# Performance work log

Measured on AMD Instinct MI355X. Metric: run time of the kernel, lower is better.

## Reference

```python
import jax, jax.numpy as jnp
import numpy as np

NW, L, D, H = 4096, 64, 128, 8
HD = D // H  # 16
NEG = -1e9


def setup_inputs() -> dict:
    key = jax.random.key(0)
    k1, k2, k3, k4, k5, k6, k7 = jax.random.split(key, 7)
    feat = jax.random.normal(k1, (NW, L, D), dtype=jnp.float32)
    pos = jax.random.normal(k2, (NW, L, D), dtype=jnp.float32) * 0.1
    # ragged window occupancy: lengths in [1, L]; mask True = padded key
    lengths = jax.random.randint(k3, (NW,), 1, L + 1)
    mask = jnp.arange(L)[None, :] >= lengths[:, None]  # [NW, L] bool
    in_proj_w = jax.random.normal(k4, (3 * D, D), dtype=jnp.float32) * 0.05
    in_proj_b = jax.random.normal(k5, (3 * D,), dtype=jnp.float32) * 0.02
    out_w = jax.random.normal(k6, (D, D), dtype=jnp.float32) * 0.05
    out_b = jax.random.normal(k7, (D,), dtype=jnp.float32) * 0.02
    return {"feat": feat, "pos": pos, "mask": mask, "in_proj_w": in_proj_w,
            "in_proj_b": in_proj_b, "out_w": out_w, "out_b": out_b}


def reference(feat, pos, mask, in_proj_w, in_proj_b, out_w, out_b):
    # q = k = feat + pos, v = feat (positional bias only on q/k, as in source)
    qk_in = feat + pos  # [NW, L, D]
    Wq, Wk, Wv = in_proj_w[:D], in_proj_w[D:2 * D], in_proj_w[2 * D:]
    bq, bk, bv = in_proj_b[:D], in_proj_b[D:2 * D], in_proj_b[2 * D:]
    q = (qk_in @ Wq.T + bq).reshape(NW, L, H, HD)
    k = (qk_in @ Wk.T + bk).reshape(NW, L, H, HD)
    v = (feat @ Wv.T + bv).reshape(NW, L, H, HD)
    scale = 1.0 / np.sqrt(HD)
    scores = jnp.einsum('nqhd,nkhd->nhqk', q, k) * scale  # [NW, H, L, L]
    scores = jnp.where(mask[:, None, None, :], NEG, scores)
    attn = jax.nn.softmax(scores, axis=-1)
    ctx = jnp.einsum('nhqk,nkhd->nqhd', attn, v).reshape(NW, L, D)
    return ctx @ out_w.T + out_b  # [NW, L, D]
```

## Files before the change

kernel.cpp:

```cpp
#include <hip/hip_runtime.h>
#include <hip/hip_bf16.h>

#define NWIN 4096
#define LW   64
#define DIM  128

typedef __attribute__((ext_vector_type(8))) short bf8;
typedef __attribute__((ext_vector_type(4))) float f4;

#define MFMA(a,b,c) __builtin_amdgcn_mfma_f32_16x16x32_bf16((a),(b),(c),0,0,0)

__device__ __forceinline__ unsigned short bfr(float f){
  __hip_bfloat16 h = __float2bfloat16(f);
  union { __hip_bfloat16 h; unsigned short u; } x; x.h = h; return x.u;
}
__device__ __forceinline__ unsigned long long pack4f(float a,float b,float c,float d){
  float2 lo2; lo2.x = a; lo2.y = b;
  float2 hi2; hi2.x = c; hi2.y = d;
  union { __hip_bfloat162 h[2]; unsigned long long u; } x;
  x.h[0] = __float22bfloat162_rn(lo2);
  x.h[1] = __float22bfloat162_rn(hi2);
  return x.u;
}
__device__ __forceinline__ bf8 mk_bf8(unsigned long long lo, unsigned long long hi){
  union { unsigned long long q[2]; bf8 v; } u; u.q[0]=lo; u.q[1]=hi; return u.v;
}

__device__ __forceinline__ bf8 frag_lds(const char* sm, int off, int rs,
                                        int rowBase, int kb, int l15, int lq){
  int row = rowBase + l15;
  int sw = (row & 7) << 4;
  unsigned long long lo = *(const unsigned long long*)(sm + off + row*rs + ((kb + 8*lq) ^ sw));
  unsigned long long hi = *(const unsigned long long*)(sm + off + row*rs + ((kb + 8*lq + 32) ^ sw));
  union { unsigned long long q[2]; bf8 v; } u; u.q[0]=lo; u.q[1]=hi; return u.v;
}

__global__ void detect_mask_kernel(const unsigned char* __restrict__ mask,
                                   int* __restrict__ ws){
  int t = blockIdx.x * blockDim.x + threadIdx.x;
  int local = 0;
  for (int i = t; i < NWIN * LW; i += gridDim.x * blockDim.x)
    if ((i & 3) && mask[i]) local = 1;
  if (local) atomicOr(ws, 1);
}

__global__ void wfrag_kernel(const float* __restrict__ in_w,
                             const float* __restrict__ ow,
                             unsigned short* __restrict__ dst){
  int t = blockIdx.x * blockDim.x + threadIdx.x;
  if (t >= 4*4*8*64*8) return;
  int e  = t & 7;
  int l  = (t >> 3) & 63;
  int nt = (t >> 9) & 7;
  int kt = (t >> 12) & 3;
  int p  = t >> 14;
  int k = kt*32 + 4*(l >> 4) + (e & 3) + 16*(e >> 2);
  int n = nt*16 + (l & 15);
  float v = (p < 3) ? in_w[(p*128 + n)*128 + k] : ow[n*128 + k];
  dst[t] = bfr(v);
}

__launch_bounds__(256, 4)
__global__ void win_attn_mfma(const float* __restrict__ feat,
                              const float* __restrict__ pos,
                              const float* __restrict__ in_b,
                              const float* __restrict__ ob,
                              const unsigned char* __restrict__ maskb,
                              const int* __restrict__ wsflag,
                              const unsigned short* __restrict__ wf,
                              float* __restrict__ out){
  extern __shared__ char sm[];
  const int n    = blockIdx.x;
  const int tid  = threadIdx.x;
  const int wave = tid >> 6, lane = tid & 63, l15 = lane & 15, lq = lane >> 4;

  const int B0 = 0, B1 = 16384;
  const f4 fzero = {0.f, 0.f, 0.f, 0.f};

  const float* fb = feat + (size_t)n * (LW*DIM);
  const float* pb = pos  + (size_t)n * (LW*DIM);
  #pragma unroll
  for (int it = 0; it < 8; ++it){
    int j = tid + it*256; int r = j >> 5, q = j & 31;
    float4 f = *(const float4*)(fb + r*DIM + q*4);
    float4 p = *(const float4*)(pb + r*DIM + q*4);
    int sw = (r & 7) << 4;
    *(unsigned long long*)(sm + B1 + r*256 + ((q*8) ^ sw)) = pack4f(f.x, f.y, f.z, f.w);
    *(unsigned long long*)(sm + B0 + r*256 + ((q*8) ^ sw)) =
        pack4f(f.x + p.x, f.y + p.y, f.z + p.z, f.w + p.w);
  }
  int mv = wsflag[0] ? (int)maskb[(size_t)n*LW + lane]
                     : ((const int*)maskb)[(size_t)n*LW + lane];
  unsigned long long bal = __ballot(mv != 0);
  const int len = bal ? (int)__builtin_ctzll(bal) : LW;
  float4 bq4[2], bk4[2];
  #pragma unroll
  for (int hh = 0; hh < 2; ++hh){
    int h = wave + 4*hh;
    bq4[hh] = *(const float4*)(in_b + h*16 + 4*lq);
    bk4[hh] = *(const float4*)(in_b + 128 + h*16 + 4*lq);
  }
  __syncthreads();

  unsigned long long q8lo[2][4], k8lo[2][4];
  {
    f4 qT[2][4], kT[2][4];
    #pragma unroll
    for (int hh = 0; hh < 2; ++hh)
      #pragma unroll
      for (int nt = 0; nt < 4; ++nt){ qT[hh][nt] = fzero; kT[hh][nt] = fzero; }
    #pragma unroll
    for (int kt = 0; kt < 4; ++kt){
      bf8 wq[2], wk[2];
      #pragma unroll
      for (int hh = 0; hh < 2; ++hh){
        int h = wave + 4*hh;
        wq[hh] = *(const bf8*)(wf + (size_t)(((0*4 + kt)*8 + h)*64 + lane)*8);
        wk[hh] = *(const bf8*)(wf + (size_t)(((1*4 + kt)*8 + h)*64 + lane)*8);
      }
      bf8 x[4];
      #pragma unroll
      for (int nt = 0; nt < 4; ++nt)
        x[nt] = frag_lds(sm, B0, 256, nt*16, kt*64, l15, lq);
      #pragma unroll
      for (int hh = 0; hh < 2; ++hh)
        #pragma unroll
        for (int nt = 0; nt < 4; ++nt){
          qT[hh][nt] = MFMA(wq[hh], x[nt], qT[hh][nt]);
          kT[hh][nt] = MFMA(wk[hh], x[nt], kT[hh][nt]);
        }
    }
    #pragma unroll
    for (int hh = 0; hh < 2; ++hh)
      #pragma unroll
      for (int nt = 0; nt < 4; ++nt){
        q8lo[hh][nt] = pack4f((qT[hh][nt][0] + bq4[hh].x) * 0.25f,
                              (qT[hh][nt][1] + bq4[hh].y) * 0.25f,
                              (qT[hh][nt][2] + bq4[hh].z) * 0.25f,
                              (qT[hh][nt][3] + bq4[hh].w) * 0.25f);
        k8lo[hh][nt] = pack4f(kT[hh][nt][0] + bk4[hh].x,
                              kT[hh][nt][1] + bk4[hh].y,
                              kT[hh][nt][2] + bk4[hh].z,
                              kT[hh][nt][3] + bk4[hh].w);
      }
  }

  f4 aV[2][4];
  #pragma unroll
  for (int g = 0; g < 2; ++g)
    #pragma unroll
    for (int nt = 0; nt < 4; ++nt) aV[g][nt] = fzero;
  #pragma unroll
  for (int kt = 0; kt < 4; ++kt){
    bf8 wv[2];
    #pragma unroll
    for (int g = 0; g < 2; ++g){
      int mt = wave + 4*g;
      wv[g] = *(const bf8*)(wf + (size_t)(((2*4 + kt)*8 + mt)*64 + lane)*8);
    }
    bf8 xf[4];
    #pragma unroll
    for (int nt = 0; nt < 4; ++nt)
      xf[nt] = frag_lds(sm, B1, 256, nt*16, kt*64, l15, lq);
    #pragma unroll
    for (int g = 0; g < 2; ++g)
      #pragma unroll
      for (int nt = 0; nt < 4; ++nt)
        aV[g][nt] = MFMA(wv[g], xf[nt], aV[g][nt]);
  }
  __syncthreads();

  #pragma unroll
  for (int g = 0; g < 2; ++g){
    int mt = wave + 4*g;
    #pragma unroll
    for (int r = 0; r < 4; ++r){
      int dim = mt*16 + 4*lq + r;
      float bv_ = in_b[256 + dim];
      #pragma unroll
      for (int nt = 0; nt < 4; ++nt){
        int col = nt*16 + l15;
        *(unsigned short*)(sm + B0 + dim*128 + ((col*2) ^ ((dim&7)<<4))) =
            bfr(aV[g][nt][r] + bv_);
      }
    }
  }

  const unsigned long long qhi = (lq == 0) ? 0x3f80ull : 0ull;
  unsigned long long khi[4];
  #pragma unroll
  for (int mt = 0; mt < 4; ++mt){
    float mval = (mt*16 + l15 < len) ? 0.f : -1e9f;
    khi[mt] = (lq == 0) ? (unsigned long long)bfr(mval) : 0ull;
  }

  #pragma unroll
  for (int hh = 0; hh < 2; ++hh){
    int h = wave + 4*hh;
    bf8 av0 = frag_lds(sm, B0, 128, h*16, 0,  l15, lq);
    bf8 av1 = frag_lds(sm, B0, 128, h*16, 64, l15, lq);
    #pragma unroll
    for (int nh = 0; nh < 2; ++nh){
      f4 s[4][2];
      __builtin_amdgcn_s_setprio(1);
      #pragma unroll
      for (int mt = 0; mt < 4; ++mt)
        #pragma unroll
        for (int j = 0; j < 2; ++j)
          s[mt][j] = MFMA(mk_bf8(k8lo[hh][mt], khi[mt]),
                          mk_bf8(q8lo[hh][2*nh + j], qhi), fzero);
      __builtin_amdgcn_s_setprio(0);
      float inv[2];
      #pragma unroll
      for (int j = 0; j < 2; ++j){
        float ss = 0.f;
        #pragma unroll
        for (int mt = 0; mt < 4; ++mt)
          #pragma unroll
          for (int r = 0; r < 4; ++r){
            float p = __expf(s[mt][j][r]);
            s[mt][j][r] = p;
            ss += p;
          }
        ss += __shfl_xor(ss, 16);
        ss += __shfl_xor(ss, 32);
        inv[j] = __builtin_amdgcn_rcpf(ss);
      }
      bf8 pb_[2][2];
      #pragma unroll
      for (int kt = 0; kt < 2; ++kt)
        #pragma unroll
        for (int j = 0; j < 2; ++j){
          unsigned long long lo = pack4f(s[2*kt  ][j][0], s[2*kt  ][j][1],
                                         s[2*kt  ][j][2], s[2*kt  ][j][3]);
          unsigned long long hi = pack4f(s[2*kt+1][j][0], s[2*kt+1][j][1],
                                         s[2*kt+1][j][2], s[2*kt+1][j][3]);
          union { unsigned long long q[2]; bf8 v; } u; u.q[0]=lo; u.q[1]=hi;
          pb_[kt][j] = u.v;
        }
      __builtin_amdgcn_s_setprio(1);
      #pragma unroll
      for (int j = 0; j < 2; ++j){
        f4 c = fzero;
        c = MFMA(av0, pb_[0][j], c);
        c = MFMA(av1, pb_[1][j], c);
        int row = (2*nh + j)*16 + l15;
        unsigned long long w = pack4f(c[0]*inv[j], c[1]*inv[j],
                                      c[2]*inv[j], c[3]*inv[j]);
        *(unsigned long long*)(sm + B1 + row*256 +
            ((32*h + 8*lq) ^ ((row&7)<<4))) = w;
      }
      __builtin_amdgcn_s_setprio(0);
    }
  }
  __syncthreads();

  {
    f4 acc[4][2];
    #pragma unroll
    for (int mt = 0; mt < 4; ++mt)
      #pragma unroll
      for (int g = 0; g < 2; ++g) acc[mt][g] = fzero;
    #pragma unroll
    for (int kt = 0; kt < 4; ++kt){
      bf8 b[2];
      #pragma unroll
      for (int g = 0; g < 2; ++g){
        int nt = wave*2 + g;
        b[g] = *(const bf8*)(wf + (size_t)(((3*4 + kt)*8 + nt)*64 + lane)*8);
      }
      bf8 a[4];
      #pragma unroll
      for (int mt = 0; mt < 4; ++mt)
        a[mt] = frag_lds(sm, B1, 256, mt*16, kt*64, l15, lq);
      #pragma unroll
      for (int g = 0; g < 2; ++g)
        #pragma unroll
        for (int mt = 0; mt < 4; ++mt)
          acc[mt][g] = MFMA(a[mt], b[g], acc[mt][g]);
    }
    float* op = out + (size_t)n * (LW*DIM);
    #pragma unroll
    for (int g = 0; g < 2; ++g){
      int nt = wave*2 + g;
      float bias = ob[nt*16 + l15];
      #pragma unroll
      for (int mt = 0; mt < 4; ++mt)
        #pragma unroll
        for (int r = 0; r < 4; ++r){
          int row = mt*16 + 4*lq + r;
          op[row*DIM + nt*16 + l15] = acc[mt][g][r] + bias;
        }
    }
  }
}

extern "C" void kernel_launch(void* const* d_in, const int* in_sizes, int n_in,
                              void* d_out, int out_size, void* d_ws, size_t ws_size,
                              hipStream_t stream){
  const float* feat = (const float*)d_in[0];
  const float* pos  = (const float*)d_in[1];
  const unsigned char* mask = (const unsigned char*)d_in[2];
  const float* in_w = (const float*)d_in[3];
  const float* in_b = (const float*)d_in[4];
  const float* ow   = (const float*)d_in[5];
  const float* ob   = (const float*)d_in[6];
  float* out = (float*)d_out;
  int* wsI = (int*)d_ws;
  unsigned short* wf = (unsigned short*)((char*)d_ws + 32768);

  hipMemsetAsync(d_ws, 0, 4, stream);
  detect_mask_kernel<<<64, 256, 0, stream>>>(mask, wsI);
  wfrag_kernel<<<(4*4*8*64*8 + 255)/256, 256, 0, stream>>>(in_w, ow, wf);
  win_attn_mfma<<<NWIN, 256, 32768, stream>>>(feat, pos, in_b, ob, mask, wsI, wf, out);
}
```

Before: 150.4 us.

## Split Q/K projections and shrink softmax tiles to cut registers for higher occupancy

```diff
diff --git a/kernel.cpp b/kernel.cpp
--- a/kernel.cpp
+++ b/kernel.cpp
@@ -60,7 +60,7 @@
   dst[t] = bfr(v);
 }
 
-__launch_bounds__(256, 4)
+__launch_bounds__(256, 5)
 __global__ void win_attn_mfma(const float* __restrict__ feat,
                               const float* __restrict__ pos,
                               const float* __restrict__ in_b,
@@ -93,29 +93,58 @@
                      : ((const int*)maskb)[(size_t)n*LW + lane];
   unsigned long long bal = __ballot(mv != 0);
   const int len = bal ? (int)__builtin_ctzll(bal) : LW;
-  float4 bq4[2], bk4[2];
-  #pragma unroll
-  for (int hh = 0; hh < 2; ++hh){
-    int h = wave + 4*hh;
-    bq4[hh] = *(const float4*)(in_b + h*16 + 4*lq);
-    bk4[hh] = *(const float4*)(in_b + 128 + h*16 + 4*lq);
-  }
   __syncthreads();
 
+  const float QSCALE = 0.25f * 1.4426950408889634f;
   unsigned long long q8lo[2][4], k8lo[2][4];
   {
-    f4 qT[2][4], kT[2][4];
+    f4 qT[2][4];
     #pragma unroll
     for (int hh = 0; hh < 2; ++hh)
       #pragma unroll
-      for (int nt = 0; nt < 4; ++nt){ qT[hh][nt] = fzero; kT[hh][nt] = fzero; }
+      for (int nt = 0; nt < 4; ++nt) qT[hh][nt] = fzero;
     #pragma unroll
     for (int kt = 0; kt < 4; ++kt){
-      bf8 wq[2], wk[2];
+      bf8 wq[2];
       #pragma unroll
       for (int hh = 0; hh < 2; ++hh){
         int h = wave + 4*hh;
         wq[hh] = *(const bf8*)(wf + (size_t)(((0*4 + kt)*8 + h)*64 + lane)*8);
+      }
+      bf8 x[4];
+      #pragma unroll
+      for (int nt = 0; nt < 4; ++nt)
+        x[nt] = frag_lds(sm, B0, 256, nt*16, kt*64, l15, lq);
+      #pragma unroll
+      for (int hh = 0; hh < 2; ++hh)
+        #pragma unroll
+        for (int nt = 0; nt < 4; ++nt)
+          qT[hh][nt] = MFMA(wq[hh], x[nt], qT[hh][nt]);
+    }
+    #pragma unroll
+    for (int hh = 0; hh < 2; ++hh){
+      int h = wave + 4*hh;
+      float4 bq4 = *(const float4*)(in_b + h*16 + 4*lq);
+      #pragma unroll
+      for (int nt = 0; nt < 4; ++nt)
+        q8lo[hh][nt] = pack4f((qT[hh][nt][0] + bq4.x) * QSCALE,
+                              (qT[hh][nt][1] + bq4.y) * QSCALE,
+                              (qT[hh][nt][2] + bq4.z) * QSCALE,
+                              (qT[hh][nt][3] + bq4.w) * QSCALE);
+    }
+  }
+  {
+    f4 kT[2][4];
+    #pragma unroll
+    for (int hh = 0; hh < 2; ++hh)
+      #pragma unroll
+      for (int nt = 0; nt < 4; ++nt) kT[hh][nt] = fzero;
+    #pragma unroll
+    for (int kt = 0; kt < 4; ++kt){
+      bf8 wk[2];
+      #pragma unroll
+      for (int hh = 0; hh < 2; ++hh){
+        int h = wave + 4*hh;
         wk[hh] = *(const bf8*)(wf + (size_t)(((1*4 + kt)*8 + h)*64 + lane)*8);
       }
       bf8 x[4];
@@ -125,24 +154,20 @@
       #pragma unroll
       for (int hh = 0; hh < 2; ++hh)
         #pragma unroll
-        for (int nt = 0; nt < 4; ++nt){
-          qT[hh][nt] = MFMA(wq[hh], x[nt], qT[hh][nt]);
+        for (int nt = 0; nt < 4; ++nt)
           kT[hh][nt] = MFMA(wk[hh], x[nt], kT[hh][nt]);
-        }
-    }
-    #pragma unroll
-    for (int hh = 0; hh < 2; ++hh)
-      #pragma unroll
-      for (int nt = 0; nt < 4; ++nt){
-        q8lo[hh][nt] = pack4f((qT[hh][nt][0] + bq4[hh].x) * 0.25f,
-                              (qT[hh][nt][1] + bq4[hh].y) * 0.25f,
-                              (qT[hh][nt][2] + bq4[hh].z) * 0.25f,
-                              (qT[hh][nt][3] + bq4[hh].w) * 0.25f);
-        k8lo[hh][nt] = pack4f(kT[hh][nt][0] + bk4[hh].x,
-                              kT[hh][nt][1] + bk4[hh].y,
-                              kT[hh][nt][2] + bk4[hh].z,
-                              kT[hh][nt][3] + bk4[hh].w);
-      }
+    }
+    #pragma unroll
+    for (int hh = 0; hh < 2; ++hh){
+      int h = wave + 4*hh;
+      float4 bk4 = *(const float4*)(in_b + 128 + h*16 + 4*lq);
+      #pragma unroll
+      for (int nt = 0; nt < 4; ++nt)
+        k8lo[hh][nt] = pack4f(kT[hh][nt][0] + bk4.x,
+                              kT[hh][nt][1] + bk4.y,
+                              kT[hh][nt][2] + bk4.z,
+                              kT[hh][nt][3] + bk4.w);
+    }
   }
 
   f4 aV[2][4];
@@ -186,12 +211,12 @@
     }
   }
 
-  const unsigned long long qhi = (lq == 0) ? 0x3f80ull : 0ull;
-  unsigned long long khi[4];
+  const unsigned qhi = (lq == 0) ? 0x3f80u : 0u;
+  unsigned khi[4];
   #pragma unroll
   for (int mt = 0; mt < 4; ++mt){
     float mval = (mt*16 + l15 < len) ? 0.f : -1e9f;
-    khi[mt] = (lq == 0) ? (unsigned long long)bfr(mval) : 0ull;
+    khi[mt] = (lq == 0) ? (unsigned)bfr(mval) : 0u;
   }
 
   #pragma unroll
@@ -200,57 +225,39 @@
     bf8 av0 = frag_lds(sm, B0, 128, h*16, 0,  l15, lq);
     bf8 av1 = frag_lds(sm, B0, 128, h*16, 64, l15, lq);
     #pragma unroll
-    for (int nh = 0; nh < 2; ++nh){
-      f4 s[4][2];
+    for (int j = 0; j < 4; ++j){
+      f4 s[4];
       __builtin_amdgcn_s_setprio(1);
       #pragma unroll
       for (int mt = 0; mt < 4; ++mt)
-        #pragma unroll
-        for (int j = 0; j < 2; ++j)
-          s[mt][j] = MFMA(mk_bf8(k8lo[hh][mt], khi[mt]),
-                          mk_bf8(q8lo[hh][2*nh + j], qhi), fzero);
+        s[mt] = MFMA(mk_bf8(k8lo[hh][mt], (unsigned long long)khi[mt]),
+                     mk_bf8(q8lo[hh][j], (unsigned long long)qhi), fzero);
       __builtin_amdgcn_s_setprio(0);
-      float inv[2];
-      #pragma unroll
-      for (int j = 0; j < 2; ++j){
-        float ss = 0.f;
-        #pragma unroll
-        for (int mt = 0; mt < 4; ++mt)
-          #pragma unroll
-          for (int r = 0; r < 4; ++r){
-            float p = __expf(s[mt][j][r]);
-            s[mt][j][r] = p;
-            ss += p;
-          }
-        ss += __shfl_xor(ss, 16);
-        ss += __shfl_xor(ss, 32);
-        inv[j] = __builtin_amdgcn_rcpf(ss);
-      }
-      bf8 pb_[2][2];
-      #pragma unroll
-      for (int kt = 0; kt < 2; ++kt)
-        #pragma unroll
-        for (int j = 0; j < 2; ++j){
-          unsigned long long lo = pack4f(s[2*kt  ][j][0], s[2*kt  ][j][1],
-                                         s[2*kt  ][j][2], s[2*kt  ][j][3]);
-          unsigned long long hi = pack4f(s[2*kt+1][j][0], s[2*kt+1][j][1],
-                                         s[2*kt+1][j][2], s[2*kt+1][j][3]);
-          union { unsigned long long q[2]; bf8 v; } u; u.q[0]=lo; u.q[1]=hi;
-          pb_[kt][j] = u.v;
+      float ss = 0.f;
+      #pragma unroll
+      for (int mt = 0; mt < 4; ++mt)
+        #pragma unroll
+        for (int r = 0; r < 4; ++r){
+          float p = __builtin_amdgcn_exp2f(s[mt][r]);
+          s[mt][r] = p;
+          ss += p;
         }
+      ss += __shfl_xor(ss, 16);
+      ss += __shfl_xor(ss, 32);
+      float inv = __builtin_amdgcn_rcpf(ss);
+      bf8 pb0 = mk_bf8(pack4f(s[0][0], s[0][1], s[0][2], s[0][3]),
+                       pack4f(s[1][0], s[1][1], s[1][2], s[1][3]));
+      bf8 pb1 = mk_bf8(pack4f(s[2][0], s[2][1], s[2][2], s[2][3]),
+                       pack4f(s[3][0], s[3][1], s[3][2], s[3][3]));
       __builtin_amdgcn_s_setprio(1);
-      #pragma unroll
-      for (int j = 0; j < 2; ++j){
-        f4 c = fzero;
-        c = MFMA(av0, pb_[0][j], c);
-        c = MFMA(av1, pb_[1][j], c);
-        int row = (2*nh + j)*16 + l15;
-        unsigned long long w = pack4f(c[0]*inv[j], c[1]*inv[j],
-                                      c[2]*inv[j], c[3]*inv[j]);
-        *(unsigned long long*)(sm + B1 + row*256 +
-            ((32*h + 8*lq) ^ ((row&7)<<4))) = w;
-      }
+      f4 c = fzero;
+      c = MFMA(av0, pb0, c);
+      c = MFMA(av1, pb1, c);
       __builtin_amdgcn_s_setprio(0);
+      int row = j*16 + l15;
+      unsigned long long w = pack4f(c[0]*inv, c[1]*inv, c[2]*inv, c[3]*inv);
+      *(unsigned long long*)(sm + B1 + row*256 +
+          ((32*h + 8*lq) ^ ((row&7)<<4))) = w;
     }
   }
   __syncthreads();
```

After: 215.4 us. 43.2% more time.
